# Performance work log

Measured on AMD Instinct MI355X. Metric: run time of the kernel, lower is better.

Reference implementation:

```python
import jax, jax.numpy as jnp
import numpy as np

LAMBDA = 0.5
TAU = 1.0
EPS = 1e-8  # torch F.cosine_similarity eps

B, D = 8192, 1024


def setup_inputs() -> dict:
    key = jax.random.key(0)
    k1, k2, k3, k4 = jax.random.split(key, 4)
    return {
        "student_query_emb": jax.random.normal(k1, (B, D), dtype=jnp.float32),
        "student_passage_emb": jax.random.normal(k2, (B, D), dtype=jnp.float32),
        "teacher_query_emb": jax.random.normal(k3, (B, D), dtype=jnp.float32),
        "teacher_passage_emb": jax.random.normal(k4, (B, D), dtype=jnp.float32),
    }


def _mse(a, b):
    d = a - b
    return jnp.mean(d * d)


def _retrieval_loss(q, p):
    # cosine sim = (q . p) / max(||q|| * ||p||, eps); normalize then matmul
    # (avoids the [B,B,D] broadcast intermediate of the torch version)
    qn = q / jnp.maximum(jnp.linalg.norm(q, axis=-1, keepdims=True), EPS)
    pn = p / jnp.maximum(jnp.linalg.norm(p, axis=-1, keepdims=True), EPS)
    logits = jnp.einsum("bd,cd->bc", qn, pn) / TAU  # [B, B]
    # cross-entropy with labels = arange(B): pick the diagonal log-prob
    logprobs = jax.nn.log_softmax(logits, axis=-1)
    return -jnp.mean(jnp.diagonal(logprobs))


def reference(student_query_emb, student_passage_emb, teacher_query_emb, teacher_passage_emb):
    distill = 0.5 * (_mse(student_query_emb, teacher_query_emb)
                     + _mse(student_passage_emb, teacher_passage_emb))
    retrieval = _retrieval_loss(student_query_emb, student_passage_emb)
    return LAMBDA * distill + (1.0 - LAMBDA) * retrieval
```

## Files before the change

kernel.cpp:

```cpp
#include <hip/hip_runtime.h>
#include <hip/hip_bf16.h>

typedef unsigned short u16;
typedef unsigned char u8;
typedef float f32x4 __attribute__((ext_vector_type(4)));
typedef int int4v __attribute__((ext_vector_type(4)));
typedef int int8v __attribute__((ext_vector_type(8)));

#define B_ROWS 8192
#define D_DIM  1024
#define FP8_SCALE 16.0f
#define ACC_UNSCALE (1.0f/256.0f)


__global__ void __launch_bounds__(256) prep_kernel(
    const float* __restrict__ sq, const float* __restrict__ sp,
    const float* __restrict__ tq, const float* __restrict__ tp,
    int* __restrict__ qn, int* __restrict__ pn,
    float* __restrict__ ppq, float* __restrict__ ppp, float* __restrict__ ppd)
{
    const int wave = threadIdx.x >> 6;
    const int l    = threadIdx.x & 63;
    const int r    = blockIdx.x * 4 + wave;
    const size_t rb4 = (size_t)r * (D_DIM / 4);

    const float4* Q4 = (const float4*)sq + rb4;
    const float4* P4 = (const float4*)sp + rb4;
    const float4* A4 = (const float4*)tq + rb4;
    const float4* B4 = (const float4*)tp + rb4;

    float4 qv[4], pv[4];
    float sq2 = 0.f, sp2 = 0.f, dq = 0.f, dp = 0.f, qp = 0.f;
    #pragma unroll
    for (int j = 0; j < 4; ++j) {
        const int idx = j * 64 + l;
        float4 q = Q4[idx], p = P4[idx], a = A4[idx], b = B4[idx];
        qv[j] = q; pv[j] = p;
        sq2 += q.x*q.x + q.y*q.y + q.z*q.z + q.w*q.w;
        sp2 += p.x*p.x + p.y*p.y + p.z*p.z + p.w*p.w;
        float dx = q.x-a.x, dy = q.y-a.y, dz = q.z-a.z, dw = q.w-a.w;
        dq += dx*dx + dy*dy + dz*dz + dw*dw;
        dx = p.x-b.x; dy = p.y-b.y; dz = p.z-b.z; dw = p.w-b.w;
        dp += dx*dx + dy*dy + dz*dz + dw*dw;
        qp += q.x*p.x + q.y*p.y + q.z*p.z + q.w*p.w;
    }

    #pragma unroll
    for (int m = 1; m <= 32; m <<= 1) {
        sq2 += __shfl_xor(sq2, m);
        sp2 += __shfl_xor(sp2, m);
        dq  += __shfl_xor(dq, m);
        dp  += __shfl_xor(dp, m);
        qp  += __shfl_xor(qp, m);
    }

    const float rq = 1.0f / fmaxf(sqrtf(sq2), 1e-8f);
    const float rp = 1.0f / fmaxf(sqrtf(sp2), 1e-8f);

    if (l == 0) {
        ppq[r] = dq;
        ppp[r] = dp;
        ppd[r] = qp * rq * rp;
    }

    const float fq = rq * FP8_SCALE;
    const float fp = rp * FP8_SCALE;
    int* qrow = qn + (size_t)r * (D_DIM / 4);
    int* prow = pn + (size_t)r * (D_DIM / 4);
    #pragma unroll
    for (int j = 0; j < 4; ++j) {
        const int idx = j * 64 + l;
        int pk = __builtin_amdgcn_cvt_pk_fp8_f32(qv[j].x * fq, qv[j].y * fq, 0, false);
        pk     = __builtin_amdgcn_cvt_pk_fp8_f32(qv[j].z * fq, qv[j].w * fq, pk, true);
        qrow[idx] = pk;
        pk = __builtin_amdgcn_cvt_pk_fp8_f32(pv[j].x * fp, pv[j].y * fp, 0, false);
        pk = __builtin_amdgcn_cvt_pk_fp8_f32(pv[j].z * fp, pv[j].w * fp, pk, true);
        prow[idx] = pk;
    }
}

union Frag { int8v v8; struct { int4v lo, hi; } h; };

__global__ void __launch_bounds__(512, 2) gemm_rowsum_kernel(
    const u8* __restrict__ Q, const u8* __restrict__ P,
    float* __restrict__ gpart)
{
    __shared__ u8 smA[2][256 * 128];
    __shared__ u8 smB[2][256 * 128];

    const int tid  = threadIdx.x;
    const int wave = tid >> 6;
    const int lane = tid & 63;
    const int wm   = wave >> 2;
    const int wn   = wave & 3;
    const int bm   = blockIdx.y;
    const int bn   = blockIdx.x;

    const int srow   = tid >> 3;
    const int schunk = (tid & 7) ^ (srow & 7);
    const u8* Ag = Q + (size_t)(bm * 256 + srow) * D_DIM + schunk * 16;
    const u8* Bg = P + (size_t)(bn * 256 + srow) * D_DIM + schunk * 16;
    const int ldsw = wave * 1024;

#define STAGE_A(b, rbase, k0)                                                  \
    __builtin_amdgcn_global_load_lds(                                          \
        (const __attribute__((address_space(1))) void*)(Ag + (size_t)(rbase) * D_DIM + (k0)), \
        (__attribute__((address_space(3))) void*)(&smA[b][(rbase) * 128] + ldsw), 16, 0, 0)
#define STAGE_B(b, rbase, k0)                                                  \
    __builtin_amdgcn_global_load_lds(                                          \
        (const __attribute__((address_space(1))) void*)(Bg + (size_t)(rbase) * D_DIM + (k0)), \
        (__attribute__((address_space(3))) void*)(&smB[b][(rbase) * 128] + ldsw), 16, 0, 0)

    const int quad = lane >> 4;
    const int rw   = lane & 15;
    const int r7   = lane & 7;
    const int off_lo = ((2 * quad) ^ r7) * 16;
    const int off_hi = ((2 * quad + 1) ^ r7) * 16;
    const int arow_base = (wm * 128 + rw) * 128;
    const int brow_base = (wn * 64  + rw) * 128;

    f32x4 acc[8][4];
    #pragma unroll
    for (int i = 0; i < 8; ++i)
        #pragma unroll
        for (int j = 0; j < 4; ++j)
            acc[i][j] = (f32x4){0.f, 0.f, 0.f, 0.f};

    STAGE_A(0, 0, 0);   STAGE_A(0, 64, 0);   STAGE_A(0, 128, 0);   STAGE_A(0, 192, 0);
    STAGE_B(0, 0, 0);   STAGE_B(0, 64, 0);   STAGE_B(0, 128, 0);   STAGE_B(0, 192, 0);
    STAGE_A(1, 0, 128); STAGE_A(1, 64, 128); STAGE_A(1, 128, 128); STAGE_A(1, 192, 128);
    STAGE_B(1, 0, 128); STAGE_B(1, 64, 128);

#define SB0 __builtin_amdgcn_sched_barrier(0);
#define WAITL(n) asm volatile("s_waitcnt lgkmcnt(" #n ")" ::: "memory"); SB0

#define READ_AF(mi)                                                            \
    af[mi].h.lo = *(const int4v*)(sA_ + arow_base + (mi) * 2048 + off_lo);     \
    af[mi].h.hi = *(const int4v*)(sA_ + arow_base + (mi) * 2048 + off_hi);
#define READ_BF(ni)                                                            \
    bf[ni].h.lo = *(const int4v*)(sB_ + brow_base + (ni) * 2048 + off_lo);     \
    bf[ni].h.hi = *(const int4v*)(sB_ + brow_base + (ni) * 2048 + off_hi);

#define MFMA1(mi, ni)                                                          \
    acc[mi][ni] = __builtin_amdgcn_mfma_scale_f32_16x16x128_f8f6f4(            \
        af[mi].v8, bf[ni].v8, acc[mi][ni],                                     \
        0, 0, 0, 0x7f7f7f7f, 0, 0x7f7f7f7f);

#define KSTEP(t, DO_B1, DO_T2, VMN)                                            \
  {                                                                            \
    constexpr int cur = (t) & 1;                                               \
    const u8* sA_ = &smA[cur][0];                                              \
    const u8* sB_ = &smB[cur][0];                                              \
    Frag af[8], bf[4];                                                         \
                  \
    if (DO_B1) { STAGE_B(cur ^ 1, 128, ((t) + 1) * 128);                       \
                 STAGE_B(cur ^ 1, 192, ((t) + 1) * 128); }                     \
    asm volatile("s_waitcnt vmcnt(" #VMN ")" ::: "memory");                    \
    __builtin_amdgcn_s_barrier();                                              \
    SB0                                                                        \
                                             \
    READ_BF(0) READ_BF(1) READ_AF(0)                                           \
    READ_AF(1) READ_AF(2) READ_AF(3)                                           \
    WAITL(6)                                         \
    __builtin_amdgcn_s_setprio(1);                                             \
    MFMA1(0, 0) MFMA1(0, 1)                                                    \
    __builtin_amdgcn_s_setprio(0);                                             \
    READ_BF(2) READ_BF(3) READ_AF(4)                                           \
    WAITL(6)                                         \
    __builtin_amdgcn_s_setprio(1);                                             \
    MFMA1(1, 0) MFMA1(1, 1) MFMA1(2, 0) MFMA1(2, 1) MFMA1(3, 0) MFMA1(3, 1)    \
    __builtin_amdgcn_s_setprio(0);                                             \
    READ_AF(5) READ_AF(6) READ_AF(7)                                           \
    WAITL(6)                                             \
    __builtin_amdgcn_s_setprio(1);                                             \
    MFMA1(0, 2) MFMA1(0, 3) MFMA1(1, 2) MFMA1(1, 3)                            \
    MFMA1(2, 2) MFMA1(2, 3) MFMA1(3, 2) MFMA1(3, 3)                            \
    MFMA1(4, 0) MFMA1(4, 1)                                                    \
    __builtin_amdgcn_s_setprio(0);                                             \
    WAITL(0)             \
    __builtin_amdgcn_s_barrier();                                              \
    SB0                                                                        \
                    \
    if (DO_T2) { STAGE_A(cur, 0,   ((t) + 2) * 128);                           \
                 STAGE_A(cur, 64,  ((t) + 2) * 128);                           \
                 STAGE_A(cur, 128, ((t) + 2) * 128);                           \
                 STAGE_A(cur, 192, ((t) + 2) * 128);                           \
                 STAGE_B(cur, 0,   ((t) + 2) * 128);                           \
                 STAGE_B(cur, 64,  ((t) + 2) * 128); }                         \
    __builtin_amdgcn_s_setprio(1);                                             \
    MFMA1(4, 2) MFMA1(4, 3)                                                    \
    MFMA1(5, 0) MFMA1(5, 1) MFMA1(5, 2) MFMA1(5, 3)                            \
    MFMA1(6, 0) MFMA1(6, 1) MFMA1(6, 2) MFMA1(6, 3)                            \
    MFMA1(7, 0) MFMA1(7, 1) MFMA1(7, 2) MFMA1(7, 3)                            \
    __builtin_amdgcn_s_setprio(0);                                             \
  }

    KSTEP(0, true,  true,  8)
    KSTEP(1, true,  true,  8)
    KSTEP(2, true,  true,  8)
    KSTEP(3, true,  true,  8)
    KSTEP(4, true,  true,  8)
    KSTEP(5, true,  true,  8)
    KSTEP(6, true,  false, 8)
    KSTEP(7, false, false, 0)

#undef KSTEP
#undef MFMA1
#undef READ_AF
#undef READ_BF
#undef WAITL
#undef SB0
#undef STAGE_A
#undef STAGE_B

    float esum[8][4];
    #pragma unroll
    for (int mi = 0; mi < 8; ++mi)
        #pragma unroll
        for (int r = 0; r < 4; ++r) {
            float s = 0.f;
            #pragma unroll
            for (int ni = 0; ni < 4; ++ni)
                s += __expf(acc[mi][ni][r] * ACC_UNSCALE);
            esum[mi][r] = s;
        }
    #pragma unroll
    for (int m = 1; m <= 8; m <<= 1)
        #pragma unroll
        for (int mi = 0; mi < 8; ++mi)
            #pragma unroll
            for (int r = 0; r < 4; ++r)
                esum[mi][r] += __shfl_xor(esum[mi][r], m);

    if (rw == 0) {
        float* dst = gpart + (size_t)(bn * 4 + wn) * B_ROWS
                   + bm * 256 + wm * 128;
        #pragma unroll
        for (int mi = 0; mi < 8; ++mi)
            #pragma unroll
            for (int r = 0; r < 4; ++r)
                dst[mi * 16 + quad * 4 + r] = esum[mi][r];
    }
}

__global__ void __launch_bounds__(256) reduce_kernel(
    const float* __restrict__ gpart,
    const float* __restrict__ ppq, const float* __restrict__ ppp,
    const float* __restrict__ ppd, float4* __restrict__ bpart)
{
    const int t = threadIdx.x;
    const int r = blockIdx.x * 256 + t;
    float s = 0.f;
    #pragma unroll 8
    for (int j = 0; j < 128; ++j) s += gpart[(size_t)j * B_ROWS + r];
    float ls = logf(s);
    float v2 = ppq[r], v3 = ppp[r], v4 = ppd[r];
    #pragma unroll
    for (int m = 1; m <= 32; m <<= 1) {
        ls += __shfl_xor(ls, m);
        v2 += __shfl_xor(v2, m);
        v3 += __shfl_xor(v3, m);
        v4 += __shfl_xor(v4, m);
    }
    __shared__ float red[4][4];
    if ((t & 63) == 0) {
        red[t >> 6][0] = ls; red[t >> 6][1] = v2;
        red[t >> 6][2] = v3; red[t >> 6][3] = v4;
    }
    __syncthreads();
    if (t == 0) {
        float4 o;
        o.x = red[0][0] + red[1][0] + red[2][0] + red[3][0];
        o.y = red[0][1] + red[1][1] + red[2][1] + red[3][1];
        o.z = red[0][2] + red[1][2] + red[2][2] + red[3][2];
        o.w = red[0][3] + red[1][3] + red[2][3] + red[3][3];
        bpart[blockIdx.x] = o;
    }
}

__global__ void __launch_bounds__(64) finalize_kernel(
    const float4* __restrict__ bpart, float* __restrict__ out)
{
    const int t = threadIdx.x;
    float4 v = (t < 32) ? bpart[t] : (float4){0.f, 0.f, 0.f, 0.f};
    #pragma unroll
    for (int m = 1; m <= 16; m <<= 1) {
        v.x += __shfl_xor(v.x, m);
        v.y += __shfl_xor(v.y, m);
        v.z += __shfl_xor(v.z, m);
        v.w += __shfl_xor(v.w, m);
    }
    if (t == 0) {
        const float inv_bd = 1.0f / ((float)B_ROWS * (float)D_DIM);
        float distill   = 0.5f * (v.y + v.z) * inv_bd;
        float retrieval = (v.x - v.w) / (float)B_ROWS;
        out[0] = 0.5f * distill + 0.5f * retrieval;
    }
}

extern "C" void kernel_launch(void* const* d_in, const int* in_sizes, int n_in,
                              void* d_out, int out_size, void* d_ws, size_t ws_size,
                              hipStream_t stream) {
    const float* sq = (const float*)d_in[0];
    const float* sp = (const float*)d_in[1];
    const float* tq = (const float*)d_in[2];
    const float* tp = (const float*)d_in[3];

    char* ws = (char*)d_ws;
    float*  ppq   = (float*)(ws);
    float*  ppp   = (float*)(ws + 32768);
    float*  ppd   = (float*)(ws + 65536);
    float4* bpart = (float4*)(ws + 98304);
    float*  gpart = (float*)(ws + 131072);
    int*    qn    = (int*)(ws + 131072 + (size_t)128 * B_ROWS * 4);
    int*    pn    = (int*)((char*)qn + (size_t)B_ROWS * D_DIM);

    prep_kernel<<<B_ROWS / 4, 256, 0, stream>>>(sq, sp, tq, tp, qn, pn, ppq, ppp, ppd);
    gemm_rowsum_kernel<<<dim3(32, 32), 512, 0, stream>>>((const u8*)qn, (const u8*)pn, gpart);
    reduce_kernel<<<32, 256, 0, stream>>>(gpart, ppq, ppp, ppd, bpart);
    finalize_kernel<<<1, 64, 0, stream>>>(bpart, (float*)d_out);
}
```

Before: 231.6 us.

## Use 4 waves with 128x128 per-wave tiles in FP8 GEMM rowsum kernel

```diff
diff --git a/kernel.cpp b/kernel.cpp
--- a/kernel.cpp
+++ b/kernel.cpp
@@ -81,7 +81,7 @@
 
 union Frag { int8v v8; struct { int4v lo, hi; } h; };
 
-__global__ void __launch_bounds__(512, 2) gemm_rowsum_kernel(
+__global__ void __launch_bounds__(256, 1) gemm_rowsum_kernel(
     const u8* __restrict__ Q, const u8* __restrict__ P,
     float* __restrict__ gpart)
 {
@@ -91,8 +91,8 @@
     const int tid  = threadIdx.x;
     const int wave = tid >> 6;
     const int lane = tid & 63;
-    const int wm   = wave >> 2;
-    const int wn   = wave & 3;
+    const int wm   = wave >> 1;
+    const int wn   = wave & 1;
     const int bm   = blockIdx.y;
     const int bn   = blockIdx.x;
 
@@ -111,25 +111,31 @@
         (const __attribute__((address_space(1))) void*)(Bg + (size_t)(rbase) * D_DIM + (k0)), \
         (__attribute__((address_space(3))) void*)(&smB[b][(rbase) * 128] + ldsw), 16, 0, 0)
 
+#define STAGE_ALL(b, k0)                                                       \
+    STAGE_A(b, 0,   k0); STAGE_A(b, 32,  k0); STAGE_A(b, 64,  k0);             \
+    STAGE_A(b, 96,  k0); STAGE_A(b, 128, k0); STAGE_A(b, 160, k0);             \
+    STAGE_A(b, 192, k0); STAGE_A(b, 224, k0);                                  \
+    STAGE_B(b, 0,   k0); STAGE_B(b, 32,  k0); STAGE_B(b, 64,  k0);             \
+    STAGE_B(b, 96,  k0); STAGE_B(b, 128, k0); STAGE_B(b, 160, k0);             \
+    STAGE_B(b, 192, k0); STAGE_B(b, 224, k0);
+
     const int quad = lane >> 4;
     const int rw   = lane & 15;
     const int r7   = lane & 7;
     const int off_lo = ((2 * quad) ^ r7) * 16;
     const int off_hi = ((2 * quad + 1) ^ r7) * 16;
     const int arow_base = (wm * 128 + rw) * 128;
-    const int brow_base = (wn * 64  + rw) * 128;
-
-    f32x4 acc[8][4];
+    const int brow_base = (wn * 128 + rw) * 128;
+
+    f32x4 acc[8][8];
     #pragma unroll
     for (int i = 0; i < 8; ++i)
         #pragma unroll
-        for (int j = 0; j < 4; ++j)
+        for (int j = 0; j < 8; ++j)
             acc[i][j] = (f32x4){0.f, 0.f, 0.f, 0.f};
 
-    STAGE_A(0, 0, 0);   STAGE_A(0, 64, 0);   STAGE_A(0, 128, 0);   STAGE_A(0, 192, 0);
-    STAGE_B(0, 0, 0);   STAGE_B(0, 64, 0);   STAGE_B(0, 128, 0);   STAGE_B(0, 192, 0);
-    STAGE_A(1, 0, 128); STAGE_A(1, 64, 128); STAGE_A(1, 128, 128); STAGE_A(1, 192, 128);
-    STAGE_B(1, 0, 128); STAGE_B(1, 64, 128);
+    STAGE_ALL(0, 0)
+    STAGE_ALL(1, 128)
 
 #define SB0 __builtin_amdgcn_sched_barrier(0);
 #define WAITL(n) asm volatile("s_waitcnt lgkmcnt(" #n ")" ::: "memory"); SB0
@@ -146,63 +152,67 @@
         af[mi].v8, bf[ni].v8, acc[mi][ni],                                     \
         0, 0, 0, 0x7f7f7f7f, 0, 0x7f7f7f7f);
 
-#define KSTEP(t, DO_B1, DO_T2, VMN)                                            \
+#define KSTEP(t, DO_T2, VMN)                                                   \
   {                                                                            \
     constexpr int cur = (t) & 1;                                               \
     const u8* sA_ = &smA[cur][0];                                              \
     const u8* sB_ = &smB[cur][0];                                              \
-    Frag af[8], bf[4];                                                         \
-                  \
-    if (DO_B1) { STAGE_B(cur ^ 1, 128, ((t) + 1) * 128);                       \
-                 STAGE_B(cur ^ 1, 192, ((t) + 1) * 128); }                     \
+    Frag af[8], bf[8];                                                         \
+         \
     asm volatile("s_waitcnt vmcnt(" #VMN ")" ::: "memory");                    \
     __builtin_amdgcn_s_barrier();                                              \
     SB0                                                                        \
-                                             \
-    READ_BF(0) READ_BF(1) READ_AF(0)                                           \
-    READ_AF(1) READ_AF(2) READ_AF(3)                                           \
-    WAITL(6)                                         \
+                                                              \
+    READ_BF(0) READ_BF(1) READ_AF(0) READ_AF(1)                                \
+    SB0                                                                        \
+                                                                   \
+    READ_AF(2) READ_AF(3) READ_BF(2) READ_BF(3)                                \
+    WAITL(8)                                        \
     __builtin_amdgcn_s_setprio(1);                                             \
-    MFMA1(0, 0) MFMA1(0, 1)                                                    \
+    MFMA1(0, 0) MFMA1(0, 1) MFMA1(1, 0) MFMA1(1, 1)                            \
     __builtin_amdgcn_s_setprio(0);                                             \
-    READ_BF(2) READ_BF(3) READ_AF(4)                                           \
-    WAITL(6)                                         \
+                                                                   \
+    READ_AF(4) READ_AF(5) READ_BF(4) READ_BF(5)                                \
+    WAITL(8)                                        \
     __builtin_amdgcn_s_setprio(1);                                             \
-    MFMA1(1, 0) MFMA1(1, 1) MFMA1(2, 0) MFMA1(2, 1) MFMA1(3, 0) MFMA1(3, 1)    \
-    __builtin_amdgcn_s_setprio(0);                                             \
-    READ_AF(5) READ_AF(6) READ_AF(7)                                           \
-    WAITL(6)                                             \
-    __builtin_amdgcn_s_setprio(1);                                             \
+    MFMA1(2, 0) MFMA1(2, 1) MFMA1(3, 0) MFMA1(3, 1)                            \
     MFMA1(0, 2) MFMA1(0, 3) MFMA1(1, 2) MFMA1(1, 3)                            \
     MFMA1(2, 2) MFMA1(2, 3) MFMA1(3, 2) MFMA1(3, 3)                            \
-    MFMA1(4, 0) MFMA1(4, 1)                                                    \
     __builtin_amdgcn_s_setprio(0);                                             \
-    WAITL(0)             \
+                                                                   \
+    READ_AF(6) READ_AF(7) READ_BF(6) READ_BF(7)                                \
+    WAITL(8)                                        \
+    __builtin_amdgcn_s_setprio(1);                                             \
+    MFMA1(4, 0) MFMA1(4, 1) MFMA1(4, 2) MFMA1(4, 3)                            \
+    MFMA1(5, 0) MFMA1(5, 1) MFMA1(5, 2) MFMA1(5, 3)                            \
+    MFMA1(0, 4) MFMA1(0, 5) MFMA1(1, 4) MFMA1(1, 5)                            \
+    MFMA1(2, 4) MFMA1(2, 5) MFMA1(3, 4) MFMA1(3, 5)                            \
+    MFMA1(4, 4) MFMA1(4, 5) MFMA1(5, 4) MFMA1(5, 5)                            \
+    __builtin_amdgcn_s_setprio(0);                                             \
+    WAITL(0)                      \
     __builtin_amdgcn_s_barrier();                                              \
     SB0                                                                        \
-                    \
-    if (DO_T2) { STAGE_A(cur, 0,   ((t) + 2) * 128);                           \
-                 STAGE_A(cur, 64,  ((t) + 2) * 128);                           \
-                 STAGE_A(cur, 128, ((t) + 2) * 128);                           \
-                 STAGE_A(cur, 192, ((t) + 2) * 128);                           \
-                 STAGE_B(cur, 0,   ((t) + 2) * 128);                           \
-                 STAGE_B(cur, 64,  ((t) + 2) * 128); }                         \
+               \
+    if (DO_T2) { STAGE_ALL(cur, ((t) + 2) * 128) }                             \
     __builtin_amdgcn_s_setprio(1);                                             \
-    MFMA1(4, 2) MFMA1(4, 3)                                                    \
-    MFMA1(5, 0) MFMA1(5, 1) MFMA1(5, 2) MFMA1(5, 3)                            \
     MFMA1(6, 0) MFMA1(6, 1) MFMA1(6, 2) MFMA1(6, 3)                            \
+    MFMA1(6, 4) MFMA1(6, 5) MFMA1(6, 6) MFMA1(6, 7)                            \
     MFMA1(7, 0) MFMA1(7, 1) MFMA1(7, 2) MFMA1(7, 3)                            \
+    MFMA1(7, 4) MFMA1(7, 5) MFMA1(7, 6) MFMA1(7, 7)                            \
+    MFMA1(0, 6) MFMA1(0, 7) MFMA1(1, 6) MFMA1(1, 7)                            \
+    MFMA1(2, 6) MFMA1(2, 7) MFMA1(3, 6) MFMA1(3, 7)                            \
+    MFMA1(4, 6) MFMA1(4, 7) MFMA1(5, 6) MFMA1(5, 7)                            \
     __builtin_amdgcn_s_setprio(0);                                             \
   }
 
-    KSTEP(0, true,  true,  8)
-    KSTEP(1, true,  true,  8)
-    KSTEP(2, true,  true,  8)
-    KSTEP(3, true,  true,  8)
-    KSTEP(4, true,  true,  8)
-    KSTEP(5, true,  true,  8)
-    KSTEP(6, true,  false, 8)
-    KSTEP(7, false, false, 0)
+    KSTEP(0, true,  16)
+    KSTEP(1, true,  16)
+    KSTEP(2, true,  16)
+    KSTEP(3, true,  16)
+    KSTEP(4, true,  16)
+    KSTEP(5, true,  16)
+    KSTEP(6, false, 16)
+    KSTEP(7, false, 0)
 
 #undef KSTEP
 #undef MFMA1
@@ -210,36 +220,44 @@
 #undef READ_BF
 #undef WAITL
 #undef SB0
+#undef STAGE_ALL
 #undef STAGE_A
 #undef STAGE_B
 
-    float esum[8][4];
-    #pragma unroll
-    for (int mi = 0; mi < 8; ++mi)
-        #pragma unroll
-        for (int r = 0; r < 4; ++r) {
-            float s = 0.f;
-            #pragma unroll
-            for (int ni = 0; ni < 4; ++ni)
-                s += __expf(acc[mi][ni][r] * ACC_UNSCALE);
-            esum[mi][r] = s;
-        }
-    #pragma unroll
-    for (int m = 1; m <= 8; m <<= 1)
+    float esum[2][8][4];
+    #pragma unroll
+    for (int h = 0; h < 2; ++h)
         #pragma unroll
         for (int mi = 0; mi < 8; ++mi)
             #pragma unroll
-            for (int r = 0; r < 4; ++r)
-                esum[mi][r] += __shfl_xor(esum[mi][r], m);
+            for (int r = 0; r < 4; ++r) {
+                float s = 0.f;
+                #pragma unroll
+                for (int ni = 0; ni < 4; ++ni)
+                    s += __expf(acc[mi][h * 4 + ni][r] * ACC_UNSCALE);
+                esum[h][mi][r] = s;
+            }
+    #pragma unroll
+    for (int m = 1; m <= 8; m <<= 1)
+        #pragma unroll
+        for (int h = 0; h < 2; ++h)
+            #pragma unroll
+            for (int mi = 0; mi < 8; ++mi)
+                #pragma unroll
+                for (int r = 0; r < 4; ++r)
+                    esum[h][mi][r] += __shfl_xor(esum[h][mi][r], m);
 
     if (rw == 0) {
-        float* dst = gpart + (size_t)(bn * 4 + wn) * B_ROWS
-                   + bm * 256 + wm * 128;
         #pragma unroll
-        for (int mi = 0; mi < 8; ++mi)
+        for (int h = 0; h < 2; ++h) {
+            float* dst = gpart + (size_t)(bn * 4 + wn * 2 + h) * B_ROWS
+                       + bm * 256 + wm * 128;
             #pragma unroll
-            for (int r = 0; r < 4; ++r)
-                dst[mi * 16 + quad * 4 + r] = esum[mi][r];
+            for (int mi = 0; mi < 8; ++mi)
+                #pragma unroll
+                for (int r = 0; r < 4; ++r)
+                    dst[mi * 16 + quad * 4 + r] = esum[h][mi][r];
+        }
     }
 }
 
@@ -316,7 +334,7 @@
     int*    pn    = (int*)((char*)qn + (size_t)B_ROWS * D_DIM);
 
     prep_kernel<<<B_ROWS / 4, 256, 0, stream>>>(sq, sp, tq, tp, qn, pn, ppq, ppp, ppd);
-    gemm_rowsum_kernel<<<dim3(32, 32), 512, 0, stream>>>((const u8*)qn, (const u8*)pn, gpart);
+    gemm_rowsum_kernel<<<dim3(32, 32), 256, 0, stream>>>((const u8*)qn, (const u8*)pn, gpart);
     reduce_kernel<<<32, 256, 0, stream>>>(gpart, ppq, ppp, ppd, bpart);
     finalize_kernel<<<1, 64, 0, stream>>>(bpart, (float*)d_out);
 }
```

Result: slower. 271.6 us (+17.3%).
